# Performance work log

Measured on AMD Instinct MI355X. Metric: run time of the kernel, lower is better.

The kernel has to match this reference:

```python
import jax, jax.numpy as jnp
import numpy as np

N_ENT, N_REL, H, DEG, TOPK = 150000, 500, 128, 32, 10


def setup_inputs() -> dict:
    key = jax.random.key(0)
    ks = jax.random.split(key, 8)
    return {
        "ent_emb": jax.random.normal(ks[0], (N_ENT, H), jnp.float32),
        "rel_emb": jax.random.normal(ks[1], (N_REL, H), jnp.float32),
        "W": jax.random.normal(ks[2], (H, H), jnp.float32) * 0.1,
        "W_r": jax.random.normal(ks[3], (H, H), jnp.float32) * 0.1,
        "a": jax.random.normal(ks[4], (3 * H, 1), jnp.float32) * 0.1,
        "neigh_w": jax.random.normal(ks[5], (H, H), jnp.float32) * 0.1,
        "src": jax.random.randint(ks[6], (N_ENT, DEG), 0, N_ENT),      # src node of each in-edge per dst
        "rel_id": jax.random.randint(ks[7], (N_ENT, DEG), 0, N_REL),   # relation id per edge
    }


def reference(ent_emb, rel_emb, W, W_r, a, neigh_w, src, rel_id):
    # node / relation projections
    h_node = ent_emb @ W                    # [N_ENT, H]
    h_rel = rel_emb @ W_r                   # [N_REL, H]
    # split attention vector: leaky_relu([h_src|h_dst|r] @ a) == leaky_relu(h_src@a1 + h_dst@a2 + r@a3)
    a1, a2, a3 = a[:H, 0], a[H:2 * H, 0], a[2 * H:, 0]
    s_src = h_node @ a1                     # [N_ENT]
    s_dst = h_node @ a2                     # [N_ENT]
    s_rel = h_rel @ a3                      # [N_REL]

    # edge scores on full graph; dst of row i is node i
    score = jax.nn.leaky_relu(s_src[src] + s_dst[:, None] + s_rel[rel_id], 0.2)  # [N_ENT, DEG]

    # top-k incoming edges per destination (dgl.sampling.select_topk, edge_dir='in')
    _, top_idx = jax.lax.top_k(score, TOPK)                 # [N_ENT, TOPK]
    src_k = jnp.take_along_axis(src, top_idx, axis=1)       # [N_ENT, TOPK]
    rel_k = jnp.take_along_axis(rel_id, top_idx, axis=1)

    # recompute attention on sampled subgraph + edge softmax per destination
    e = jax.nn.leaky_relu(s_src[src_k] + s_dst[:, None] + s_rel[rel_k], 0.2)     # [N_ENT, TOPK]
    attn = jax.nn.softmax(e, axis=1)

    # composition (add) of gathered src features with relation features, weighted scatter-sum
    comp = h_node[src_k] + h_rel[rel_k]                     # [N_ENT, TOPK, H]
    neigh = jnp.einsum('nkh,nk->nh', comp, attn)            # weighted sum over in-edges

    out = jnp.tanh(neigh @ neigh_w)                         # bn=None, dropout=eval identity
    return out
```

## Files before the change

### kernel.cpp

```cpp
#include <hip/hip_runtime.h>
#include <hip/hip_bf16.h>
#include <math.h>

#define N_ENT 150000
#define N_REL 500
#define H     128
#define DEG   32
#define TOPK  10

typedef unsigned short ushort_t;
typedef unsigned int   uint_t;
typedef __attribute__((ext_vector_type(8))) short short8;
typedef __attribute__((ext_vector_type(4))) float f32x4;
typedef __attribute__((ext_vector_type(2))) float f32x2;

__device__ inline ushort_t f2bf(float x) {
    __hip_bfloat16 h = __float2bfloat16(x);
    return *reinterpret_cast<ushort_t*>(&h);
}
__device__ inline float bf2f(ushort_t u) {
    uint_t v = ((uint_t)u) << 16;
    return *reinterpret_cast<float*>(&v);
}
__device__ inline f32x2 unpk2(uint_t u) {
    uint_t lo = u << 16;
    uint_t hi = u & 0xFFFF0000u;
    f32x2 r;
    r.x = *reinterpret_cast<float*>(&lo);
    r.y = *reinterpret_cast<float*>(&hi);
    return r;
}
__device__ inline float dot4(float4 a, float4 b) {
    return a.x * b.x + a.y * b.y + a.z * b.z + a.w * b.w;
}
__device__ inline float fast_tanh(float x) {
    float e = __expf(2.f * x);
    return 1.f - 2.f * __builtin_amdgcn_rcpf(e + 1.f);
}

__global__ __launch_bounds__(128) void precompute_small(
    const float* __restrict__ W, const float* __restrict__ Wr,
    const float* __restrict__ nw, const float* __restrict__ a,
    float* __restrict__ M, float* __restrict__ M2,
    float* __restrict__ v1, float* __restrict__ v2, float* __restrict__ u3)
{
    int j = threadIdx.x;
    if (blockIdx.x < H) {
        int r = blockIdx.x;
        float m = 0.f, m2 = 0.f;
        for (int t = 0; t < H; ++t) {
            float x = nw[t * H + j];
            m  += W [r * H + t] * x;
            m2 += Wr[r * H + t] * x;
        }
        M [r * H + j] = m;
        M2[r * H + j] = m2;
    } else {
        int h = j;
        float s1 = 0.f, s2 = 0.f, s3 = 0.f;
        for (int t = 0; t < H; ++t) {
            s1 += W [h * H + t] * a[t];
            s2 += W [h * H + t] * a[H + t];
            s3 += Wr[h * H + t] * a[2 * H + t];
        }
        v1[h] = s1; v2[h] = s2; u3[h] = s3;
    }
}

__global__ __launch_bounds__(64) void bfrag_build(
    const float* __restrict__ M, ushort_t* __restrict__ Bhi,
    ushort_t* __restrict__ Blo)
{
    int b = blockIdx.x;
    int c = b >> 2, tt = b & 3;
    int l = threadIdx.x;
    int n  = c * 16 + (l & 15);
    int k0 = tt * 32 + (l >> 4) * 8;
    #pragma unroll
    for (int j = 0; j < 8; ++j) {
        float x = M[(k0 + j) * H + n];
        ushort_t h = f2bf(x);
        Bhi[(size_t)(b * 64 + l) * 8 + j] = h;
        Blo[(size_t)(b * 64 + l) * 8 + j] = f2bf(x - bf2f(h));
    }
}

__global__ __launch_bounds__(128) void rel_transform(
    const float* __restrict__ rel, const float* __restrict__ M2,
    const float* __restrict__ u3, ushort_t* __restrict__ Rb,
    float* __restrict__ srel)
{
    __shared__ float red[H];
    int r = blockIdx.x, j = threadIdx.x;
    float acc = 0.f;
    for (int h = 0; h < H; ++h)
        acc += rel[r * H + h] * M2[h * H + j];
    Rb[r * H + j] = f2bf(acc);
    red[j] = rel[r * H + j] * u3[j];
    __syncthreads();
    for (int s = 64; s > 0; s >>= 1) {
        if (j < s) red[j] += red[j + s];
        __syncthreads();
    }
    if (j == 0) srel[r] = red[0];
}

__global__ __launch_bounds__(256) void ent_transform3(
    const float* __restrict__ ent, const ushort_t* __restrict__ Bhi,
    const ushort_t* __restrict__ Blo, const float* __restrict__ v1,
    const float* __restrict__ v2, ushort_t* __restrict__ Gb,
    float* __restrict__ ssrc, float* __restrict__ sdst)
{
    const int t    = threadIdx.x;
    const int w    = t >> 6;
    const int l    = t & 63;
    const int m    = l & 15;
    const int quad = l >> 4;
    const long blockRow = (long)blockIdx.x * 128;
    const long waveRow  = blockRow + (long)w * 32;

    float4 v1a[4], v1b[4], v2a[4], v2b[4];
    #pragma unroll
    for (int tt = 0; tt < 4; ++tt) {
        const float* p1 = v1 + tt * 32 + quad * 8;
        const float* p2 = v2 + tt * 32 + quad * 8;
        v1a[tt] = *(const float4*)p1; v1b[tt] = *(const float4*)(p1 + 4);
        v2a[tt] = *(const float4*)p2; v2b[tt] = *(const float4*)(p2 + 4);
    }

    short8 Ahi[2][4], Alo[2][4];
    float p1s[2] = {0.f, 0.f}, p2s[2] = {0.f, 0.f};
    #pragma unroll
    for (int s = 0; s < 2; ++s) {
        long row = waveRow + s * 16 + m;
        long rc  = row < N_ENT ? row : (N_ENT - 1);
        const float* rp = ent + rc * H;
        #pragma unroll
        for (int tt = 0; tt < 4; ++tt) {
            float4 e0 = *(const float4*)(rp + tt * 32 + quad * 8);
            float4 e1 = *(const float4*)(rp + tt * 32 + quad * 8 + 4);
            p1s[s] += dot4(e0, v1a[tt]) + dot4(e1, v1b[tt]);
            p2s[s] += dot4(e0, v2a[tt]) + dot4(e1, v2b[tt]);
            float x[8] = {e0.x, e0.y, e0.z, e0.w, e1.x, e1.y, e1.z, e1.w};
            #pragma unroll
            for (int j = 0; j < 8; ++j) {
                ushort_t h = f2bf(x[j]);
                Ahi[s][tt][j] = (short)h;
                Alo[s][tt][j] = (short)f2bf(x[j] - bf2f(h));
            }
        }
    }
    #pragma unroll
    for (int s = 0; s < 2; ++s) {
        p1s[s] += __shfl_xor(p1s[s], 16); p1s[s] += __shfl_xor(p1s[s], 32);
        p2s[s] += __shfl_xor(p2s[s], 16); p2s[s] += __shfl_xor(p2s[s], 32);
    }
    if (quad == 0) {
        #pragma unroll
        for (int s = 0; s < 2; ++s) {
            long row = waveRow + s * 16 + m;
            if (row < N_ENT) { ssrc[row] = p1s[s]; sdst[row] = p2s[s]; }
        }
    }

    for (int c = 0; c < 8; ++c) {
        short8 bh[4], bl[4];
        #pragma unroll
        for (int tt = 0; tt < 4; ++tt) {
            size_t off = (size_t)((c * 4 + tt) * 64 + l) * 8;
            bh[tt] = *(const short8*)(Bhi + off);
            bl[tt] = *(const short8*)(Blo + off);
        }
        f32x4 acc0 = {0.f, 0.f, 0.f, 0.f}, acc1 = {0.f, 0.f, 0.f, 0.f};
        #pragma unroll
        for (int tt = 0; tt < 4; ++tt) {
            acc0 = __builtin_amdgcn_mfma_f32_16x16x32_bf16(bh[tt], Ahi[0][tt], acc0, 0, 0, 0);
            acc0 = __builtin_amdgcn_mfma_f32_16x16x32_bf16(bh[tt], Alo[0][tt], acc0, 0, 0, 0);
            acc0 = __builtin_amdgcn_mfma_f32_16x16x32_bf16(bl[tt], Ahi[0][tt], acc0, 0, 0, 0);
            acc1 = __builtin_amdgcn_mfma_f32_16x16x32_bf16(bh[tt], Ahi[1][tt], acc1, 0, 0, 0);
            acc1 = __builtin_amdgcn_mfma_f32_16x16x32_bf16(bh[tt], Alo[1][tt], acc1, 0, 0, 0);
            acc1 = __builtin_amdgcn_mfma_f32_16x16x32_bf16(bl[tt], Ahi[1][tt], acc1, 0, 0, 0);
        }
        #pragma unroll
        for (int s = 0; s < 2; ++s) {
            f32x4 a = s ? acc1 : acc0;
            long row = waveRow + s * 16 + m;
            if (row < N_ENT) {
                ushort4 o;
                o.x = f2bf(a[0]); o.y = f2bf(a[1]);
                o.z = f2bf(a[2]); o.w = f2bf(a[3]);
                *(ushort4*)(Gb + (size_t)row * H + c * 16 + quad * 4) = o;
            }
        }
    }
}

__global__ __launch_bounds__(256) void gather_topk_out(
    const int* __restrict__ src, const int* __restrict__ rel_id,
    const float* __restrict__ ssrc, const float* __restrict__ sdst,
    const float* __restrict__ srel, const ushort_t* __restrict__ Gb,
    const ushort_t* __restrict__ Rb, float* __restrict__ out)
{
    const int l         = threadIdx.x & 31;
    const int halfShift = threadIdx.x & 32;
    const uint_t tie1   = (uint_t)(31 - l);
    const ushort_t* GbL = Gb + l * 4;
    const ushort_t* RbL = Rb + l * 4;
    int hw  = (blockIdx.x * blockDim.x + threadIdx.x) >> 5;
    int nhw = (gridDim.x * blockDim.x) >> 5;

    for (int i = hw; i < N_ENT; i += nhw) {
        int sidx = src   [(size_t)i * DEG + l];
        int ridx = rel_id[(size_t)i * DEG + l];
        float x   = ssrc[sidx] + sdst[i] + srel[ridx];
        float val = x >= 0.f ? x : 0.2f * x;

        uint_t ub = __builtin_bit_cast(uint_t, val);
        uint_t mk = ub ^ (uint_t)(((int)ub >> 31) | (int)0x80000000);
        unsigned long long k1 = ((unsigned long long)mk << 5) | tie1;

        int rank = 0;
        uint_t mxk = mk;
        #pragma unroll
        for (int xm = 1; xm < 32; ++xm) {
            uint_t mk2 = (uint_t)__shfl_xor((int)mk, xm, 32);
            unsigned long long k2 =
                ((unsigned long long)mk2 << 5) | (tie1 ^ (uint_t)xm);
            rank += (k2 > k1) ? 1 : 0;
            mxk = mk2 > mxk ? mk2 : mxk;
        }
        bool sel = rank < TOPK;

        uint_t mu = ((int)mxk < 0) ? (mxk ^ 0x80000000u) : ~mxk;
        float mx = *reinterpret_cast<float*>(&mu);

        float e  = sel ? __expf(val - mx) : 0.f;
        float ws = e;
        #pragma unroll
        for (int off = 1; off < 32; off <<= 1)
            ws += __shfl_xor(ws, off, 32);
        float w = e * __builtin_amdgcn_rcpf(ws);

        unsigned long long ball = __ballot(sel);
        uint_t mask = (uint_t)(ball >> halfShift);

        uint_t packed = (uint_t)sidx | ((uint_t)ridx << 18);
        uint_t pk[TOPK]; float wk[TOPK];
        #pragma unroll
        for (int k = 0; k < TOPK; ++k) {
            int lk = (int)__builtin_ctz(mask); mask &= mask - 1;
            pk[k] = (uint_t)__shfl((int)packed, lk, 32);
            wk[k] = __shfl(w, lk, 32);
        }

        uint2 gv[TOPK], rv[TOPK];
        #pragma unroll
        for (int k = 0; k < TOPK; ++k) {
            size_t s_k = pk[k] & 0x3FFFF;
            size_t r_k = pk[k] >> 18;
            gv[k] = *(const uint2*)(GbL + s_k * H);
            rv[k] = *(const uint2*)(RbL + r_k * H);
        }
        f32x2 a01 = {0.f, 0.f}, a23 = {0.f, 0.f};
        #pragma unroll
        for (int k = 0; k < TOPK; ++k) {
            float wv = wk[k];
            f32x2 g01 = unpk2(gv[k].x), g23 = unpk2(gv[k].y);
            f32x2 r01 = unpk2(rv[k].x), r23 = unpk2(rv[k].y);
            a01 += (g01 + r01) * wv;
            a23 += (g23 + r23) * wv;
        }
        float4 o;
        o.x = fast_tanh(a01.x); o.y = fast_tanh(a01.y);
        o.z = fast_tanh(a23.x); o.w = fast_tanh(a23.y);
        ((float4*)(out + (size_t)i * H))[l] = o;
    }
}

extern "C" void kernel_launch(void* const* d_in, const int* in_sizes, int n_in,
                              void* d_out, int out_size, void* d_ws, size_t ws_size,
                              hipStream_t stream) {
    const float* ent = (const float*)d_in[0];
    const float* rel = (const float*)d_in[1];
    const float* W   = (const float*)d_in[2];
    const float* Wr  = (const float*)d_in[3];
    const float* a   = (const float*)d_in[4];
    const float* nw  = (const float*)d_in[5];
    const int*   src = (const int*)d_in[6];
    const int*   rid = (const int*)d_in[7];
    float* out = (float*)d_out;

    float* ws = (float*)d_ws;
    float*    M    = ws;
    float*    M2   = M    + 16384;
    float*    v1   = M2   + 16384;
    float*    v2   = v1   + 128;
    float*    u3   = v2   + 128;
    float*    srel = u3   + 128;
    float*    ssrc = srel + 512;
    float*    sdst = ssrc + 150016;
    ushort_t* Bhi  = (ushort_t*)(sdst + 150016);
    ushort_t* Blo  = Bhi + 16384;
    ushort_t* Rb   = Blo + 16384;
    ushort_t* Gb   = Rb  + 64000;

    precompute_small<<<H + 1, H, 0, stream>>>(W, Wr, nw, a, M, M2, v1, v2, u3);
    bfrag_build    <<<32, 64, 0, stream>>>(M, Bhi, Blo);
    rel_transform  <<<N_REL, H, 0, stream>>>(rel, M2, u3, Rb, srel);
    ent_transform3 <<<(N_ENT + 127) / 128, 256, 0, stream>>>(ent, Bhi, Blo,
                                                             v1, v2, Gb, ssrc, sdst);
    gather_topk_out<<<2048, 256, 0, stream>>>(src, rid, ssrc, sdst, srel,
                                              Gb, Rb, out);
}
```

Baseline: 328.9 us.

## Prefetch next row's indices and scores; simplify softmax max and normalization

Software-pipelines the grid-stride loop so that the src/rel_id indices and the gathered s_src/s_dst/s_rel scores for the next destination row are loaded while the current row's top-k, softmax and feature gather run. The max is now taken from the rank-0 lane through a ballot and shuffle, which drops the per-shuffle max tracking. The softmax denominator is summed from the ten shuffled exponentials instead of a butterfly reduction, and normalization is applied once to the accumulator. This adds register pressure from the prefetched values, which could lower occupancy.

```diff
diff --git a/kernel.cpp b/kernel.cpp
--- a/kernel.cpp
+++ b/kernel.cpp
@@ -209,37 +209,46 @@
     int hw  = (blockIdx.x * blockDim.x + threadIdx.x) >> 5;
     int nhw = (gridDim.x * blockDim.x) >> 5;
 
-    for (int i = hw; i < N_ENT; i += nhw) {
-        int sidx = src   [(size_t)i * DEG + l];
-        int ridx = rel_id[(size_t)i * DEG + l];
-        float x   = ssrc[sidx] + sdst[i] + srel[ridx];
+    int i = hw;
+    if (i >= N_ENT) return;
+
+    int   sidx = src   [(size_t)i * DEG + l];
+    int   ridx = rel_id[(size_t)i * DEG + l];
+    float s1 = ssrc[sidx], s2 = sdst[i], s3 = srel[ridx];
+
+    while (true) {
+        const int inext = i + nhw;
+        const int ic    = inext < N_ENT ? inext : i;
+
+        const size_t off2 = (size_t)ic * DEG + l;
+        int sidx2 = src[off2];
+        int ridx2 = rel_id[off2];
+
+        float x   = s1 + s2 + s3;
         float val = x >= 0.f ? x : 0.2f * x;
-
         uint_t ub = __builtin_bit_cast(uint_t, val);
         uint_t mk = ub ^ (uint_t)(((int)ub >> 31) | (int)0x80000000);
         unsigned long long k1 = ((unsigned long long)mk << 5) | tie1;
 
         int rank = 0;
-        uint_t mxk = mk;
         #pragma unroll
         for (int xm = 1; xm < 32; ++xm) {
             uint_t mk2 = (uint_t)__shfl_xor((int)mk, xm, 32);
             unsigned long long k2 =
                 ((unsigned long long)mk2 << 5) | (tie1 ^ (uint_t)xm);
             rank += (k2 > k1) ? 1 : 0;
-            mxk = mk2 > mxk ? mk2 : mxk;
         }
         bool sel = rank < TOPK;
 
-        uint_t mu = ((int)mxk < 0) ? (mxk ^ 0x80000000u) : ~mxk;
-        float mx = *reinterpret_cast<float*>(&mu);
-
-        float e  = sel ? __expf(val - mx) : 0.f;
-        float ws = e;
-        #pragma unroll
-        for (int off = 1; off < 32; off <<= 1)
-            ws += __shfl_xor(ws, off, 32);
-        float w = e * __builtin_amdgcn_rcpf(ws);
+        float s1n = ssrc[sidx2];
+        float s2n = sdst[ic];
+        float s3n = srel[ridx2];
+
+        unsigned long long b0 = __ballot(rank == 0);
+        int l0 = (int)__builtin_ctz((uint_t)(b0 >> halfShift));
+        float mx = __shfl(val, l0, 32);
+
+        float e = sel ? __expf(val - mx) : 0.f;
 
         unsigned long long ball = __ballot(sel);
         uint_t mask = (uint_t)(ball >> halfShift);
@@ -250,17 +259,21 @@
         for (int k = 0; k < TOPK; ++k) {
             int lk = (int)__builtin_ctz(mask); mask &= mask - 1;
             pk[k] = (uint_t)__shfl((int)packed, lk, 32);
-            wk[k] = __shfl(w, lk, 32);
-        }
+            wk[k] = __shfl(e, lk, 32);
+        }
+        float ws = ((wk[0] + wk[1]) + (wk[2] + wk[3]))
+                 + ((wk[4] + wk[5]) + (wk[6] + wk[7]))
+                 + (wk[8] + wk[9]);
+        float rnorm = __builtin_amdgcn_rcpf(ws);
 
         uint2 gv[TOPK], rv[TOPK];
         #pragma unroll
-        for (int k = 0; k < TOPK; ++k) {
-            size_t s_k = pk[k] & 0x3FFFF;
-            size_t r_k = pk[k] >> 18;
-            gv[k] = *(const uint2*)(GbL + s_k * H);
-            rv[k] = *(const uint2*)(RbL + r_k * H);
-        }
+        for (int k = 0; k < TOPK; ++k)
+            gv[k] = *(const uint2*)(GbL + (size_t)(pk[k] & 0x3FFFF) * H);
+        #pragma unroll
+        for (int k = 0; k < TOPK; ++k)
+            rv[k] = *(const uint2*)(RbL + (size_t)(pk[k] >> 18) * H);
+
         f32x2 a01 = {0.f, 0.f}, a23 = {0.f, 0.f};
         #pragma unroll
         for (int k = 0; k < TOPK; ++k) {
@@ -270,10 +283,17 @@
             a01 += (g01 + r01) * wv;
             a23 += (g23 + r23) * wv;
         }
+        a01 *= rnorm; a23 *= rnorm;
+
         float4 o;
         o.x = fast_tanh(a01.x); o.y = fast_tanh(a01.y);
         o.z = fast_tanh(a23.x); o.w = fast_tanh(a23.y);
         ((float4*)(out + (size_t)i * H))[l] = o;
+
+        if (inext >= N_ENT) break;
+        i = inext;
+        sidx = sidx2; ridx = ridx2;
+        s1 = s1n; s2 = s2n; s3 = s3n;
     }
 }
 
```

After: 317.4 us. 1.04x faster.
